# Kernel optimization log

Measured on AMD Instinct MI355X. Metric: run time of the kernel, lower is better.

Reference implementation:

```python
import jax, jax.numpy as jnp
import numpy as np

B, S, D, H, DFF = 2, 4096, 768, 12, 3072
DH = D // H
EPS = 1e-6


def layer_norm(x, gamma, beta):
    # torch.std is unbiased (ddof=1); normalizer is (sigma + eps), NOT sqrt(var+eps)
    mu = jnp.mean(x, axis=-1, keepdims=True)
    sigma = jnp.sqrt(jnp.var(x, axis=-1, keepdims=True, ddof=1))
    return gamma * (x - mu) / (sigma + EPS) + beta


def setup_inputs() -> dict:
    key = jax.random.key(0)
    ks = jax.random.split(key, 12)
    sc = 1.0 / np.sqrt(D)
    inp = {
        "x": jax.random.normal(ks[0], (B, S, D), dtype=jnp.float32),
        "mask": jnp.ones((B, S, S), dtype=jnp.float32),  # multiplicative mask
        "wq": jax.random.normal(ks[1], (D, D), dtype=jnp.float32) * sc,
        "bq": jnp.zeros((D,), dtype=jnp.float32),
        "wk": jax.random.normal(ks[2], (D, D), dtype=jnp.float32) * sc,
        "bk": jnp.zeros((D,), dtype=jnp.float32),
        "wv": jax.random.normal(ks[3], (D, D), dtype=jnp.float32) * sc,
        "bv": jnp.zeros((D,), dtype=jnp.float32),
        "wo": jax.random.normal(ks[4], (D, D), dtype=jnp.float32) * sc,
        "bo": jnp.zeros((D,), dtype=jnp.float32),
        "w1": jax.random.normal(ks[5], (D, DFF), dtype=jnp.float32) * sc,
        "b1": jnp.zeros((DFF,), dtype=jnp.float32),
        "w2": jax.random.normal(ks[6], (DFF, D), dtype=jnp.float32) * (1.0 / np.sqrt(DFF)),
        "b2": jnp.zeros((D,), dtype=jnp.float32),
        "gamma1": jnp.ones((D,), dtype=jnp.float32),
        "beta1": jnp.zeros((D,), dtype=jnp.float32),
        "gamma2": jnp.ones((D,), dtype=jnp.float32),
        "beta2": jnp.zeros((D,), dtype=jnp.float32),
    }
    return inp


def reference(x, mask, wq, bq, wk, bk, wv, bv, wo, bo, w1, b1, w2, b2,
              gamma1, beta1, gamma2, beta2):
    # Pre-LN encoder layer (is_pre_layer_norm=True); dropout is identity (eval).
    l1 = layer_norm(x, gamma1, beta1)                      # [B,S,D]

    # --- multi-head self-attention ---
    q = (l1 @ wq + bq).reshape(B, S, H, DH).transpose(0, 2, 1, 3)  # [B,H,S,DH]
    k = (l1 @ wk + bk).reshape(B, S, H, DH).transpose(0, 2, 1, 3)
    v = (l1 @ wv + bv).reshape(B, S, H, DH).transpose(0, 2, 1, 3)
    scores = jnp.einsum("bhqd,bhkd->bhqk", q, k) / jnp.sqrt(jnp.float32(DH))
    scores = scores * mask[:, None, :, :]                  # multiplicative mask, pre-softmax
    attn = jax.nn.softmax(scores, axis=-1)                 # [B,H,S,S]
    ctx = jnp.einsum("bhqk,bhkd->bhqd", attn, v)           # [B,H,S,DH]
    ctx = ctx.transpose(0, 2, 1, 3).reshape(B, S, D)       # [B,S,D]
    a = ctx  # NOTE: original forward never applies out_linear in attention()... it does in forward
    a = ctx
    # MultiHeadAttention.forward returns the merged heads WITHOUT out_linear applied?
    # Re-check: forward() reshapes and returns `output` without out_linear in given code.
    x1 = x + a                                             # residual

    l2 = layer_norm(x1, gamma2, beta2)
    h = jax.nn.relu(l2 @ w1 + b1) @ w2 + b2                # FFN
    return h + x1
```

## Files before the change

kernel.cpp:

```cpp
#include <hip/hip_runtime.h>
#include <cstdint>
#include <cstddef>

#define BB   2
#define SEQ  4096
#define DD   768
#define HH   12
#define DHH  64
#define DFFN 3072
#define NTOK (BB*SEQ)

using bf16x8 = __attribute__((ext_vector_type(8))) __bf16;
using f32x4  = __attribute__((ext_vector_type(4))) float;
typedef unsigned int u32;

#define QK_SCALE 0.18033688011112042f

__device__ __forceinline__ float fast_exp2(float x) {
    return __builtin_amdgcn_exp2f(x);
}

__device__ __forceinline__ unsigned short f2bf(float f) {
    unsigned u = __float_as_uint(f);
    u = u + 0x7FFFu + ((u >> 16) & 1u);
    return (unsigned short)(u >> 16);
}
__device__ __forceinline__ unsigned short f2bf_trunc(float f) {
    return (unsigned short)(__float_as_uint(f) >> 16);
}

__device__ __forceinline__ bf16x8 ld_bf8(const unsigned short* p) {
    return *(const bf16x8*)p;
}

__device__ __forceinline__ bf16x8 pack_bf8(f32x4 a, f32x4 b) {
    union { u32 w[4]; bf16x8 v; } u;
    u.w[0] = (u32)f2bf_trunc(a[0]) | ((u32)f2bf_trunc(a[1]) << 16);
    u.w[1] = (u32)f2bf_trunc(a[2]) | ((u32)f2bf_trunc(a[3]) << 16);
    u.w[2] = (u32)f2bf_trunc(b[0]) | ((u32)f2bf_trunc(b[1]) << 16);
    u.w[3] = (u32)f2bf_trunc(b[2]) | ((u32)f2bf_trunc(b[3]) << 16);
    return u.v;
}
__device__ __forceinline__ bf16x8 vfrag(const unsigned short* lo, const unsigned short* hi) {
    union { uint2 d[2]; bf16x8 v; } u;
    u.d[0] = *(const uint2*)lo;
    u.d[1] = *(const uint2*)hi;
    return u.v;
}
__device__ __forceinline__ bf16x8 ones_bf8() {
    union { u32 w[4]; bf16x8 v; } u;
    u.w[0] = u.w[1] = u.w[2] = u.w[3] = 0x3F803F80u;
    return u.v;
}

__device__ __forceinline__ void gl_lds16(const unsigned short* g, unsigned short* l) {
    __builtin_amdgcn_global_load_lds(
        (const __attribute__((address_space(1))) u32*)(uintptr_t)(const void*)g,
        (__attribute__((address_space(3))) u32*)(uintptr_t)(void*)l,
        16, 0, 0);
}

__global__ __launch_bounds__(256) void transpose_qkv_to_bf16(
    const float* __restrict__ wq, const float* __restrict__ wk, const float* __restrict__ wv,
    const float* __restrict__ bq, const float* __restrict__ bk, const float* __restrict__ bv,
    unsigned short* __restrict__ dst, float* __restrict__ bqkv)
{
    __shared__ float tile[32][33];
    const int z = blockIdx.z;
    const float* src = (z == 0) ? wq : (z == 1 ? wk : wv);
    const float scale = (z == 0) ? QK_SCALE : 1.0f;
    unsigned short* d = dst + (size_t)z * 768 * 768;
    const int c0 = blockIdx.x * 32, r0 = blockIdx.y * 32;
    const int tx = threadIdx.x, ty = threadIdx.y;
    if (blockIdx.x == 0 && blockIdx.y == 0) {
        const float* bsrc = (z == 0) ? bq : (z == 1 ? bk : bv);
        const int tid = ty * 32 + tx;
        for (int i = tid; i < 768; i += 256)
            bqkv[z * 768 + i] = bsrc[i] * scale;
    }
#pragma unroll
    for (int i = 0; i < 32; i += 8)
        tile[ty + i][tx] = src[(size_t)(r0 + ty + i) * 768 + c0 + tx];
    __syncthreads();
#pragma unroll
    for (int i = 0; i < 32; i += 8)
        d[(size_t)(c0 + ty + i) * 768 + r0 + tx] = f2bf(scale * tile[tx][ty + i]);
}

__global__ __launch_bounds__(256) void transpose_f32_to_bf16(
    const float* __restrict__ src, unsigned short* __restrict__ dst, int R, int C, float scale)
{
    __shared__ float tile[32][33];
    const int c0 = blockIdx.x * 32, r0 = blockIdx.y * 32;
    const int tx = threadIdx.x, ty = threadIdx.y;
#pragma unroll
    for (int i = 0; i < 32; i += 8)
        tile[ty + i][tx] = src[(size_t)(r0 + ty + i) * C + c0 + tx];
    __syncthreads();
#pragma unroll
    for (int i = 0; i < 32; i += 8)
        dst[(size_t)(c0 + ty + i) * R + r0 + tx] = f2bf(scale * tile[tx][ty + i]);
}

__global__ __launch_bounds__(256) void mask_check(const float* __restrict__ mask, int* __restrict__ flag)
{
    const size_t n = (size_t)BB * SEQ * SEQ;
    const size_t stride = (size_t)gridDim.x * 1024;
    int bad = 0;
    for (size_t i = ((size_t)blockIdx.x * 256 + threadIdx.x) * 4; i < n; i += stride) {
        float4 v = *(const float4*)&mask[i];
        bad |= (v.x != 1.f) | (v.y != 1.f) | (v.z != 1.f) | (v.w != 1.f);
    }
    if (bad) atomicOr(flag, 1);
}

__global__ __launch_bounds__(256) void ln_fused(
    const float* __restrict__ x, const float* __restrict__ add,
    const float* __restrict__ gamma, const float* __restrict__ beta,
    unsigned short* __restrict__ out_ln, float* __restrict__ x1out)
{
    const int row = blockIdx.x, t = threadIdx.x;
    const size_t base = (size_t)row * DD;
    float v[3], s = 0.f, sq = 0.f;
#pragma unroll
    for (int p = 0; p < 3; ++p) {
        int idx = t + p * 256;
        float val = x[base + idx];
        if (add) val += add[base + idx];
        v[p] = val; s += val; sq += val * val;
    }
#pragma unroll
    for (int off = 1; off < 64; off <<= 1) {
        s  += __shfl_xor(s,  off);
        sq += __shfl_xor(sq, off);
    }
    __shared__ float red[8];
    const int wave = t >> 6;
    if ((t & 63) == 0) { red[wave] = s; red[4 + wave] = sq; }
    __syncthreads();
    s  = red[0] + red[1] + red[2] + red[3];
    sq = red[4] + red[5] + red[6] + red[7];
    const float mu   = s * (1.f / 768.f);
    const float var  = fmaxf((sq - 768.f * mu * mu) * (1.f / 767.f), 0.f);
    const float rstd = 1.f / (sqrtf(var) + 1e-6f);
#pragma unroll
    for (int p = 0; p < 3; ++p) {
        int idx = t + p * 256;
        if (x1out) x1out[base + idx] = v[p];
        out_ln[base + idx] = f2bf(gamma[idx] * (v[p] - mu) * rstd + beta[idx]);
    }
}

__global__ __launch_bounds__(256) void gemm_bf16(
    const unsigned short* __restrict__ A, const unsigned short* __restrict__ Bt,
    const float* __restrict__ bias, const float* __restrict__ resid,
    unsigned short* __restrict__ outB, float* __restrict__ outF,
    int M, int N, int K, int relu)
{
    __shared__ __align__(16) unsigned short As[2][128][64];
    __shared__ __align__(16) unsigned short Bs[2][128][64];
    const int tid = threadIdx.x;
    const int lane = tid & 63, wave = tid >> 6;
    const int quad = lane >> 4, l16 = lane & 15;
    const int wm = wave >> 1, wn = wave & 1;

    int wg = blockIdx.y * gridDim.x + blockIdx.x;
    const int nwg = gridDim.x * gridDim.y;
    wg = (wg & 7) * (nwg >> 3) + (wg >> 3);
    const int m0 = (wg / gridDim.x) * 128, n0 = (wg % gridDim.x) * 128;

    const f32x4 fzero = {0.f, 0.f, 0.f, 0.f};
    f32x4 acc[4][4];
#pragma unroll
    for (int i = 0; i < 4; ++i)
#pragma unroll
        for (int j = 0; j < 4; ++j) acc[i][j] = fzero;

    const int r  = tid >> 3;
    const int cg = tid & 7;

#define G_STAGE(BUF_, K0_) do {                                                       \
    _Pragma("unroll")                                                                 \
    for (int rr = 0; rr < 4; ++rr) {                                                  \
        const int row = r + rr * 32;                                                  \
        const int gc8 = (cg ^ (row & 7)) * 8;                                         \
        gl_lds16(&A [(size_t)(m0 + row) * K + (K0_) + gc8], &As[BUF_][row][cg * 8]);  \
        gl_lds16(&Bt[(size_t)(n0 + row) * K + (K0_) + gc8], &Bs[BUF_][row][cg * 8]);  \
    }                                                                                 \
} while (0)

    const int nt = K >> 6;
    G_STAGE(0, 0);

    for (int t = 0; t < nt; ++t) {
        const int cur = t & 1;
        if (t + 1 < nt) {
            G_STAGE(cur ^ 1, (t + 1) * 64);
            asm volatile("s_waitcnt vmcnt(8)" ::: "memory");
        } else {
            asm volatile("s_waitcnt vmcnt(0)" ::: "memory");
        }
        __builtin_amdgcn_s_barrier();
#pragma unroll
        for (int ks = 0; ks < 2; ++ks) {
            bf16x8 af[4], bfv[4];
#pragma unroll
            for (int i = 0; i < 4; ++i) {
                const int row = wm * 64 + i * 16 + l16;
                af[i] = ld_bf8(&As[cur][row][((ks * 4 + quad) ^ (row & 7)) * 8]);
            }
#pragma unroll
            for (int j = 0; j < 4; ++j) {
                const int row = wn * 64 + j * 16 + l16;
                bfv[j] = ld_bf8(&Bs[cur][row][((ks * 4 + quad) ^ (row & 7)) * 8]);
            }
#pragma unroll
            for (int i = 0; i < 4; ++i)
#pragma unroll
                for (int j = 0; j < 4; ++j)
                    acc[i][j] = __builtin_amdgcn_mfma_f32_16x16x32_bf16(af[i], bfv[j], acc[i][j], 0, 0, 0);
        }
        __builtin_amdgcn_s_barrier();
    }
#undef G_STAGE

#pragma unroll
    for (int i = 0; i < 4; ++i)
#pragma unroll
        for (int j = 0; j < 4; ++j)
#pragma unroll
            for (int rr = 0; rr < 4; ++rr) {
                const int gm = m0 + wm * 64 + i * 16 + quad * 4 + rr;
                const int gn = n0 + wn * 64 + j * 16 + l16;
                float v = acc[i][j][rr] + bias[gn];
                if (relu) v = fmaxf(v, 0.f);
                if (resid) v += resid[(size_t)gm * N + gn];
                if (outF) outF[(size_t)gm * N + gn] = v;
                if (outB) outB[(size_t)gm * N + gn] = f2bf(v);
            }
}

__global__ __launch_bounds__(256) void vt_extract(
    const unsigned short* __restrict__ qkv, unsigned short* __restrict__ vtg)
{
    __shared__ unsigned short tile[64][72];
    const int bh = blockIdx.x, b = bh / HH, h = bh % HH;
    const int s0 = blockIdx.y * 64;
    const int tid = threadIdx.x;
#pragma unroll
    for (int p = 0; p < 2; ++p) {
        int idx = tid + p * 256;
        int r = idx >> 3, ch8 = (idx & 7) * 8;
        *(uint4*)&tile[r][ch8] =
            *(const uint4*)&qkv[(size_t)(b * SEQ + s0 + r) * 2304 + 1536 + h * 64 + ch8];
    }
    __syncthreads();
#pragma unroll
    for (int p = 0; p < 2; ++p) {
        int idx = tid + p * 256;
        int d = idx >> 3, sc = (idx & 7) * 8;
        unsigned short tmp[8];
#pragma unroll
        for (int j = 0; j < 8; ++j) tmp[j] = tile[sc + j][d];
        *(uint4*)&vtg[((size_t)bh * 64 + d) * SEQ + s0 + sc] = *(uint4*)tmp;
    }
}

__global__ __launch_bounds__(256, 3) void flash_attn13(
    const unsigned short* __restrict__ qkv, const unsigned short* __restrict__ vtg,
    const float* __restrict__ mask, const int* __restrict__ maskflag,
    float* __restrict__ ctx)
{
    __shared__ __align__(16) unsigned short Ks[128][72];
    __shared__ __align__(16) unsigned short Vt[64][136];

    const int tid = threadIdx.x;
    const int lane = tid & 63, wave = tid >> 6;
    const int quad = lane >> 4, l16 = lane & 15;
    const int NT = SEQ / 128;

    const int wg  = blockIdx.y * 32 + blockIdx.x;
    const int swz = (wg & 7) * 96 + (wg >> 3);
    const int bh = swz >> 5, b = bh / HH, h = bh % HH;
    const int qbase = (swz & 31) * 128 + wave * 32;
    const int use_mask = *maskflag;

    bf16x8 qf[2][2];
#pragma unroll
    for (int mt = 0; mt < 2; ++mt) {
        const size_t qrow = (size_t)(b * SEQ + qbase + mt * 16 + l16) * 2304 + h * 64;
        qf[mt][0] = ld_bf8(&qkv[qrow + quad * 8]);
        qf[mt][1] = ld_bf8(&qkv[qrow + 32 + quad * 8]);
    }
    const f32x4 fzero = {0.f, 0.f, 0.f, 0.f};
    const bf16x8 vones = ones_bf8();
    f32x4 l_acc[2];
    f32x4 o[2][4];
#pragma unroll
    for (int mt = 0; mt < 2; ++mt) {
        l_acc[mt] = fzero;
#pragma unroll
        for (int r = 0; r < 4; ++r) o[mt][r] = fzero;
    }

    const float* mbase = mask + (size_t)b * SEQ * SEQ;
    const unsigned short* kgbase = qkv + (size_t)b * SEQ * 2304 + 768 + h * 64;
    const unsigned short* vgbase = vtg + (size_t)bh * 64 * SEQ;

    const int sr  = tid >> 3, sc8 = (tid & 7) * 8;
    const int vd  = tid >> 4, vc8 = (tid & 15) * 8;

#define LOAD_KV(K0_)                                                                  \
    kb0 = *(const uint4*)&kgbase[(size_t)((K0_) + sr +  0) * 2304 + sc8];             \
    kb1 = *(const uint4*)&kgbase[(size_t)((K0_) + sr + 32) * 2304 + sc8];             \
    kb2 = *(const uint4*)&kgbase[(size_t)((K0_) + sr + 64) * 2304 + sc8];             \
    kb3 = *(const uint4*)&kgbase[(size_t)((K0_) + sr + 96) * 2304 + sc8];             \
    vb0 = *(const uint4*)&vgbase[(size_t)(vd +  0) * SEQ + (K0_) + vc8];              \
    vb1 = *(const uint4*)&vgbase[(size_t)(vd + 16) * SEQ + (K0_) + vc8];              \
    vb2 = *(const uint4*)&vgbase[(size_t)(vd + 32) * SEQ + (K0_) + vc8];              \
    vb3 = *(const uint4*)&vgbase[(size_t)(vd + 48) * SEQ + (K0_) + vc8]

#define WRITE_KV()                                                                    \
    *(uint4*)&Ks[sr +  0][sc8] = kb0;                                                 \
    *(uint4*)&Ks[sr + 32][sc8] = kb1;                                                 \
    *(uint4*)&Ks[sr + 64][sc8] = kb2;                                                 \
    *(uint4*)&Ks[sr + 96][sc8] = kb3;                                                 \
    *(uint4*)&Vt[vd +  0][vc8] = vb0;                                                 \
    *(uint4*)&Vt[vd + 16][vc8] = vb1;                                                 \
    *(uint4*)&Vt[vd + 32][vc8] = vb2;                                                 \
    *(uint4*)&Vt[vd + 48][vc8] = vb3

#define QKT_TILE() do {                                                               \
    _Pragma("unroll")                                                                 \
    for (int j = 0; j < 8; ++j) {                                                     \
        bf16x8 kf0 = ld_bf8(&Ks[j * 16 + l16][quad * 8]);                             \
        bf16x8 kf1 = ld_bf8(&Ks[j * 16 + l16][32 + quad * 8]);                        \
        st[0][j] = __builtin_amdgcn_mfma_f32_16x16x32_bf16(kf0, qf[0][0], fzero, 0, 0, 0); \
        st[0][j] = __builtin_amdgcn_mfma_f32_16x16x32_bf16(kf1, qf[0][1], st[0][j], 0, 0, 0); \
        st[1][j] = __builtin_amdgcn_mfma_f32_16x16x32_bf16(kf0, qf[1][0], fzero, 0, 0, 0); \
        st[1][j] = __builtin_amdgcn_mfma_f32_16x16x32_bf16(kf1, qf[1][1], st[1][j], 0, 0, 0); \
    }                                                                                 \
} while (0)

#define PV_TILE() do {                                                                \
    _Pragma("unroll")                                                                 \
    for (int kk = 0; kk < 4; ++kk) {                                                  \
        bf16x8 pa0 = pack_bf8(st[0][2 * kk], st[0][2 * kk + 1]);                      \
        bf16x8 pa1 = pack_bf8(st[1][2 * kk], st[1][2 * kk + 1]);                      \
        l_acc[0] = __builtin_amdgcn_mfma_f32_16x16x32_bf16(pa0, vones, l_acc[0], 0, 0, 0); \
        l_acc[1] = __builtin_amdgcn_mfma_f32_16x16x32_bf16(pa1, vones, l_acc[1], 0, 0, 0); \
        _Pragma("unroll")                                                             \
        for (int v = 0; v < 4; ++v) {                                                 \
            const unsigned short* vrow = &Vt[v * 16 + l16][kk * 32 + quad * 4];       \
            bf16x8 vf = vfrag(vrow, vrow + 16);                                       \
            o[0][v] = __builtin_amdgcn_mfma_f32_16x16x32_bf16(pa0, vf, o[0][v], 0, 0, 0); \
            o[1][v] = __builtin_amdgcn_mfma_f32_16x16x32_bf16(pa1, vf, o[1][v], 0, 0, 0); \
        }                                                                             \
    }                                                                                 \
} while (0)

    {
        uint4 kb0, kb1, kb2, kb3, vb0, vb1, vb2, vb3;
        LOAD_KV(0);
        WRITE_KV();
    }

    if (!use_mask) {
        for (int t = 0; t < NT; ++t) {
            __syncthreads();
            const int kn = ((t + 1) & (NT - 1)) * 128;
            uint4 kb0, kb1, kb2, kb3, vb0, vb1, vb2, vb3;
            LOAD_KV(kn);
            f32x4 st[2][8];
            QKT_TILE();
#pragma unroll
            for (int mt = 0; mt < 2; ++mt)
#pragma unroll
                for (int j = 0; j < 8; ++j)
#pragma unroll
                    for (int r = 0; r < 4; ++r)
                        st[mt][j][r] = fast_exp2(st[mt][j][r]);
            PV_TILE();
            __syncthreads();
            if (t < NT - 1) { WRITE_KV(); }
        }
    } else {
        float l_run[2] = {0.f, 0.f};
        float m_run[2] = {-1e30f, -1e30f};
        for (int t = 0; t < NT; ++t) {
            const int k0 = t * 128;
            __syncthreads();
            const int kn = ((t + 1) & (NT - 1)) * 128;
            uint4 kb0, kb1, kb2, kb3, vb0, vb1, vb2, vb3;
            LOAD_KV(kn);
            f32x4 st[2][8];
            QKT_TILE();
#pragma unroll
            for (int mt = 0; mt < 2; ++mt) {
                const float* mrow =
                    &mbase[(size_t)(qbase + mt * 16 + l16) * SEQ + k0 + quad * 4];
#pragma unroll
                for (int j = 0; j < 8; ++j)
#pragma unroll
                    for (int r = 0; r < 4; ++r)
                        st[mt][j][r] *= mrow[j * 16 + r];
            }
#pragma unroll
            for (int mt = 0; mt < 2; ++mt) {
                float mx = st[mt][0][0];
#pragma unroll
                for (int j = 0; j < 8; ++j)
#pragma unroll
                    for (int r = 0; r < 4; ++r) mx = fmaxf(mx, st[mt][j][r]);
                mx = fmaxf(mx, __shfl_xor(mx, 16));
                mx = fmaxf(mx, __shfl_xor(mx, 32));
                const float mnew = fmaxf(m_run[mt], mx);
                const float alpha = fast_exp2(m_run[mt] - mnew);
                float ssum = 0.f;
#pragma unroll
                for (int j = 0; j < 8; ++j)
#pragma unroll
                    for (int r = 0; r < 4; ++r) {
                        st[mt][j][r] = fast_exp2(st[mt][j][r] - mnew);
                        ssum += st[mt][j][r];
                    }
                ssum += __shfl_xor(ssum, 16);
                ssum += __shfl_xor(ssum, 32);
                l_run[mt] = l_run[mt] * alpha + ssum;
                m_run[mt] = mnew;
                float aq[4];
#pragma unroll
                for (int r = 0; r < 4; ++r) aq[r] = __shfl(alpha, quad * 4 + r);
#pragma unroll
                for (int v = 0; v < 4; ++v)
#pragma unroll
                    for (int r = 0; r < 4; ++r) o[mt][v][r] *= aq[r];
            }
            PV_TILE();
            __syncthreads();
            if (t < NT - 1) { WRITE_KV(); }
        }
#pragma unroll
        for (int mt = 0; mt < 2; ++mt)
#pragma unroll
            for (int r = 0; r < 4; ++r)
                l_acc[mt][r] = __shfl(l_run[mt], quad * 4 + r);
    }
#undef LOAD_KV
#undef WRITE_KV
#undef QKT_TILE
#undef PV_TILE

#pragma unroll
    for (int mt = 0; mt < 2; ++mt)
#pragma unroll
        for (int v = 0; v < 4; ++v)
#pragma unroll
            for (int r = 0; r < 4; ++r) {
                const int row = qbase + mt * 16 + quad * 4 + r;
                ctx[(size_t)(b * SEQ + row) * DD + h * 64 + v * 16 + l16] =
                    o[mt][v][r] / l_acc[mt][r];
            }
}

extern "C" void kernel_launch(void* const* d_in, const int* in_sizes, int n_in,
                              void* d_out, int out_size, void* d_ws, size_t ws_size,
                              hipStream_t stream)
{
    (void)in_sizes; (void)n_in; (void)out_size; (void)ws_size;
    const float* x      = (const float*)d_in[0];
    const float* mask   = (const float*)d_in[1];
    const float* wq     = (const float*)d_in[2];
    const float* bq     = (const float*)d_in[3];
    const float* wk     = (const float*)d_in[4];
    const float* bk     = (const float*)d_in[5];
    const float* wv     = (const float*)d_in[6];
    const float* bv     = (const float*)d_in[7];
    const float* w1     = (const float*)d_in[10];
    const float* b1     = (const float*)d_in[11];
    const float* w2     = (const float*)d_in[12];
    const float* b2     = (const float*)d_in[13];
    const float* gamma1 = (const float*)d_in[14];
    const float* beta1  = (const float*)d_in[15];
    const float* gamma2 = (const float*)d_in[16];
    const float* beta2  = (const float*)d_in[17];
    float* out = (float*)d_out;

    char* ws = (char*)d_ws;
    size_t off = 0;
    auto take = [&](size_t bytes) -> char* {
        char* p = ws + off;
        off = (off + bytes + 255) & ~(size_t)255;
        return p;
    };
    unsigned short* wqkvT = (unsigned short*)take((size_t)2304 * 768 * 2);
    unsigned short* w1T   = (unsigned short*)take((size_t)3072 * 768 * 2);
    unsigned short* w2T   = (unsigned short*)take((size_t)768 * 3072 * 2);
    float*          bqkv  = (float*)take(2304 * 4);
    int*            mflag = (int*)take(256);
    unsigned short* l12   = (unsigned short*)take((size_t)NTOK * DD * 2);
    unsigned short* qkv   = (unsigned short*)take((size_t)NTOK * 2304 * 2);
    float*          x1    = (float*)take((size_t)NTOK * DD * 4);
    char*           big   = take((size_t)NTOK * DFFN * 2);
    float*          ctx   = (float*)big;
    unsigned short* vtg   = (unsigned short*)(big + (size_t)NTOK * DD * 4);
    unsigned short* hb    = (unsigned short*)big;

    (void)hipMemsetAsync(mflag, 0, 4, stream);
    mask_check<<<2048, 256, 0, stream>>>(mask, mflag);

    transpose_qkv_to_bf16<<<dim3(24, 24, 3), dim3(32, 8), 0, stream>>>(
        wq, wk, wv, bq, bk, bv, wqkvT, bqkv);
    transpose_f32_to_bf16<<<dim3(96, 24), dim3(32, 8), 0, stream>>>(w1, w1T, 768, 3072, 1.0f);
    transpose_f32_to_bf16<<<dim3(24, 96), dim3(32, 8), 0, stream>>>(w2, w2T, 3072, 768, 1.0f);

    ln_fused<<<NTOK, 256, 0, stream>>>(x, nullptr, gamma1, beta1, l12, nullptr);
    gemm_bf16<<<dim3(2304 / 128, NTOK / 128), 256, 0, stream>>>(
        l12, wqkvT, bqkv, nullptr, qkv, nullptr, NTOK, 2304, 768, 0);
    vt_extract<<<dim3(BB * HH, SEQ / 64), 256, 0, stream>>>(qkv, vtg);
    flash_attn13<<<dim3(SEQ / 128, BB * HH), 256, 0, stream>>>(qkv, vtg, mask, mflag, ctx);
    ln_fused<<<NTOK, 256, 0, stream>>>(x, ctx, gamma2, beta2, l12, x1);
    gemm_bf16<<<dim3(3072 / 128, NTOK / 128), 256, 0, stream>>>(
        l12, w1T, b1, nullptr, hb, nullptr, NTOK, 3072, 768, 1);
    gemm_bf16<<<dim3(768 / 128, NTOK / 128), 256, 0, stream>>>(
        hb, w2T, b2, x1, nullptr, out, NTOK, 768, 3072, 0);
}
```

Before: 558.9 us.

## Fuse V transpose into QKV GEMM epilogue and raise wave priority around MFMA

The QKV GEMM epilogue now writes the V columns directly in transposed layout (via an LDS staging buffer that reuses the GEMM shared memory), which removes the separate vt_extract kernel and its extra read of the qkv buffer. The V part of qkv is no longer written, which is fine because attention reads V only from vtg. s_setprio is also raised around the MFMA sections in both the GEMM and flash attention so that compute waves are favoured over load-issuing waves. The fused epilogue adds an LDS round trip and a block sync to the V tiles.

```diff
diff --git a/kernel.cpp b/kernel.cpp
--- a/kernel.cpp
+++ b/kernel.cpp
@@ -155,10 +155,12 @@
     const unsigned short* __restrict__ A, const unsigned short* __restrict__ Bt,
     const float* __restrict__ bias, const float* __restrict__ resid,
     unsigned short* __restrict__ outB, float* __restrict__ outF,
+    unsigned short* __restrict__ vtg,
     int M, int N, int K, int relu)
 {
-    __shared__ __align__(16) unsigned short As[2][128][64];
-    __shared__ __align__(16) unsigned short Bs[2][128][64];
+    __shared__ __align__(16) unsigned short SM[2 * 2 * 128 * 64];
+    unsigned short (* const As)[128][64] = (unsigned short (*)[128][64])SM;
+    unsigned short (* const Bs)[128][64] = (unsigned short (*)[128][64])(SM + 2 * 128 * 64);
     const int tid = threadIdx.x;
     const int lane = tid & 63, wave = tid >> 6;
     const int quad = lane >> 4, l16 = lane & 15;
@@ -201,6 +203,7 @@
             asm volatile("s_waitcnt vmcnt(0)" ::: "memory");
         }
         __builtin_amdgcn_s_barrier();
+        __builtin_amdgcn_s_setprio(1);
 #pragma unroll
         for (int ks = 0; ks < 2; ++ks) {
             bf16x8 af[4], bfv[4];
@@ -220,9 +223,39 @@
                 for (int j = 0; j < 4; ++j)
                     acc[i][j] = __builtin_amdgcn_mfma_f32_16x16x32_bf16(af[i], bfv[j], acc[i][j], 0, 0, 0);
         }
+        __builtin_amdgcn_s_setprio(0);
         __builtin_amdgcn_s_barrier();
     }
 #undef G_STAGE
+
+    if (vtg && n0 >= 1536) {
+        unsigned short* trbuf = SM;
+#pragma unroll
+        for (int j = 0; j < 4; ++j)
+#pragma unroll
+            for (int i = 0; i < 4; ++i) {
+                const int cc = wn * 64 + j * 16 + l16;
+                const int ss = wm * 64 + i * 16 + quad * 4;
+                const float bb = bias[n0 + cc];
+                uint2 p;
+                p.x = (u32)f2bf(acc[i][j][0] + bb) | ((u32)f2bf(acc[i][j][1] + bb) << 16);
+                p.y = (u32)f2bf(acc[i][j][2] + bb) | ((u32)f2bf(acc[i][j][3] + bb) << 16);
+                *(uint2*)&trbuf[cc * 136 + ss] = p;
+            }
+        __syncthreads();
+        const int b    = m0 >> 12;
+        const int srow = m0 & 4095;
+#pragma unroll
+        for (int it = 0; it < 8; ++it) {
+            const int idx = it * 256 + tid;
+            const int cc  = idx >> 4;
+            const int sc8 = (idx & 15) * 8;
+            const int hd  = n0 - 1536 + cc;
+            *(uint4*)&vtg[((size_t)(b * 768 + hd)) * SEQ + srow + sc8] =
+                *(const uint4*)&trbuf[cc * 136 + sc8];
+        }
+        return;
+    }
 
 #pragma unroll
     for (int i = 0; i < 4; ++i)
@@ -240,33 +273,7 @@
             }
 }
 
-__global__ __launch_bounds__(256) void vt_extract(
-    const unsigned short* __restrict__ qkv, unsigned short* __restrict__ vtg)
-{
-    __shared__ unsigned short tile[64][72];
-    const int bh = blockIdx.x, b = bh / HH, h = bh % HH;
-    const int s0 = blockIdx.y * 64;
-    const int tid = threadIdx.x;
-#pragma unroll
-    for (int p = 0; p < 2; ++p) {
-        int idx = tid + p * 256;
-        int r = idx >> 3, ch8 = (idx & 7) * 8;
-        *(uint4*)&tile[r][ch8] =
-            *(const uint4*)&qkv[(size_t)(b * SEQ + s0 + r) * 2304 + 1536 + h * 64 + ch8];
-    }
-    __syncthreads();
-#pragma unroll
-    for (int p = 0; p < 2; ++p) {
-        int idx = tid + p * 256;
-        int d = idx >> 3, sc = (idx & 7) * 8;
-        unsigned short tmp[8];
-#pragma unroll
-        for (int j = 0; j < 8; ++j) tmp[j] = tile[sc + j][d];
-        *(uint4*)&vtg[((size_t)bh * 64 + d) * SEQ + s0 + sc] = *(uint4*)tmp;
-    }
-}
-
-__global__ __launch_bounds__(256, 3) void flash_attn13(
+__global__ __launch_bounds__(256, 3) void flash_attn14(
     const unsigned short* __restrict__ qkv, const unsigned short* __restrict__ vtg,
     const float* __restrict__ mask, const int* __restrict__ maskflag,
     float* __restrict__ ctx)
@@ -331,6 +338,7 @@
     *(uint4*)&Vt[vd + 48][vc8] = vb3
 
 #define QKT_TILE() do {                                                               \
+    __builtin_amdgcn_s_setprio(1);                                                    \
     _Pragma("unroll")                                                                 \
     for (int j = 0; j < 8; ++j) {                                                     \
         bf16x8 kf0 = ld_bf8(&Ks[j * 16 + l16][quad * 8]);                             \
@@ -340,9 +348,11 @@
         st[1][j] = __builtin_amdgcn_mfma_f32_16x16x32_bf16(kf0, qf[1][0], fzero, 0, 0, 0); \
         st[1][j] = __builtin_amdgcn_mfma_f32_16x16x32_bf16(kf1, qf[1][1], st[1][j], 0, 0, 0); \
     }                                                                                 \
+    __builtin_amdgcn_s_setprio(0);                                                    \
 } while (0)
 
 #define PV_TILE() do {                                                                \
+    __builtin_amdgcn_s_setprio(1);                                                    \
     _Pragma("unroll")                                                                 \
     for (int kk = 0; kk < 4; ++kk) {                                                  \
         bf16x8 pa0 = pack_bf8(st[0][2 * kk], st[0][2 * kk + 1]);                      \
@@ -357,6 +367,7 @@
             o[1][v] = __builtin_amdgcn_mfma_f32_16x16x32_bf16(pa1, vf, o[1][v], 0, 0, 0); \
         }                                                                             \
     }                                                                                 \
+    __builtin_amdgcn_s_setprio(0);                                                    \
 } while (0)
 
     {
@@ -516,12 +527,11 @@
 
     ln_fused<<<NTOK, 256, 0, stream>>>(x, nullptr, gamma1, beta1, l12, nullptr);
     gemm_bf16<<<dim3(2304 / 128, NTOK / 128), 256, 0, stream>>>(
-        l12, wqkvT, bqkv, nullptr, qkv, nullptr, NTOK, 2304, 768, 0);
-    vt_extract<<<dim3(BB * HH, SEQ / 64), 256, 0, stream>>>(qkv, vtg);
-    flash_attn13<<<dim3(SEQ / 128, BB * HH), 256, 0, stream>>>(qkv, vtg, mask, mflag, ctx);
+        l12, wqkvT, bqkv, nullptr, qkv, nullptr, vtg, NTOK, 2304, 768, 0);
+    flash_attn14<<<dim3(SEQ / 128, BB * HH), 256, 0, stream>>>(qkv, vtg, mask, mflag, ctx);
     ln_fused<<<NTOK, 256, 0, stream>>>(x, ctx, gamma2, beta2, l12, x1);
     gemm_bf16<<<dim3(3072 / 128, NTOK / 128), 256, 0, stream>>>(
-        l12, w1T, b1, nullptr, hb, nullptr, NTOK, 3072, 768, 1);
+        l12, w1T, b1, nullptr, hb, nullptr, nullptr, NTOK, 3072, 768, 1);
     gemm_bf16<<<dim3(768 / 128, NTOK / 128), 256, 0, stream>>>(
-        hb, w2T, b2, x1, nullptr, out, NTOK, 768, 3072, 0);
-}
+        hb, w2T, b2, x1, nullptr, out, nullptr, NTOK, 768, 3072, 0);
+}
```

After: 588.3 us. 1.05x slower.
